# Performance work log

Measured on AMD Instinct MI355X. Metric: run time of the kernel, lower is better.

## Reference

```python
import jax, jax.numpy as jnp
import numpy as np

C0 = 0.28209479177387814
C1 = 0.4886025119029199
C2 = (1.0925484305920792, -1.0925484305920792, 0.31539156525252005,
      -1.0925484305920792, 0.5462742152960396)
EPS = 1e-6


def eval_sh_bases2(d):
    # d: [..., 3] unit directions -> [..., 9] SH basis (degree 2, svox2 convention)
    x, y, z = d[..., 0], d[..., 1], d[..., 2]
    return jnp.stack([
        jnp.full_like(x, C0),
        -C1 * y, C1 * z, -C1 * x,
        C2[0] * x * y, C2[1] * y * z,
        C2[2] * (2.0 * z * z - x * x - y * y),
        C2[3] * x * z, C2[4] * (x * x - y * y),
    ], axis=-1)


def get_sh_vals(xyz, sh_feats, invs, locs):
    # xyz: [N,3]; sh_feats: [J,9]; invs: [J,4,4]; locs: [J,3] -> weights [N,J]
    n = xyz.shape[0]
    xyz_h = jnp.concatenate([xyz, jnp.ones((n, 1), xyz.dtype)], axis=-1)  # [N,4]
    pts = jnp.einsum('jab,nb->jna', invs, xyz_h)[..., :3]  # [J,N,3]
    vd = locs[:, None, :] - pts                             # [J,N,3]
    norm = jnp.linalg.norm(vd, axis=-1)                     # [J,N]
    lengths = jnp.nan_to_num(norm)
    vd = vd / jnp.maximum(norm, 1e-12)[..., None]           # F.normalize
    sh = eval_sh_bases2(vd)                                 # [J,N,9]
    rads = jax.nn.relu(jnp.einsum('jnk,jk->jn', sh, sh_feats) + 0.5)
    rel = jax.nn.relu(1.0 - lengths / jnp.maximum(rads, EPS))
    rel = jnp.where(rads < EPS, 0.0, rel)
    return rel.T  # [N,J]


def weighted_transformation(pts, weights, transforms):
    # pts: [M,3]; weights: [M,J]; transforms: [J,4,4] (already inverse transforms,
    # if_transform_is_inv=True). Linear-blend the matrices and apply.
    wsum = weights.sum(axis=-1, keepdims=True)              # [M,1]
    wn = weights / jnp.maximum(wsum, EPS)
    T = jnp.einsum('mj,jab->mab', wn, transforms)           # [M,4,4]
    p_h = jnp.concatenate([pts, jnp.ones((pts.shape[0], 1), pts.dtype)], axis=-1)
    out = jnp.einsum('mab,mb->ma', T, p_h)[:, :3]
    return jnp.where(wsum > EPS, out, pts)                  # untouched if no weight


def setup_inputs() -> dict:
    key = jax.random.key(0)
    ks = jax.random.split(key, 5)
    B, S, J = 4096, 128, 24
    return {
        'xyz_sampled': jax.random.normal(ks[0], (B, S, 3), jnp.float32),
        'viewdirs': jax.random.normal(ks[1], (B, S, 3), jnp.float32),
        'transforms': jax.random.normal(ks[2], (J, 4, 4), jnp.float32),
        'ray_valid': jnp.ones((B, S), dtype=bool),
        'sh_feats': jax.random.normal(ks[3], (J, 9), jnp.float32),
        'locs': jax.random.normal(ks[4], (J, 3), jnp.float32),
    }


def reference(xyz_sampled, viewdirs, transforms, ray_valid, sh_feats, locs):
    shape = xyz_sampled.shape
    x = xyz_sampled.reshape(-1, 3)
    n = x.shape[0]
    tmp = jnp.concatenate([x, (xyz_sampled - viewdirs).reshape(-1, 3)], axis=0)  # [2N,3]
    w = get_sh_vals(x, sh_feats, transforms, locs)          # [N,J]
    w2 = jnp.concatenate([w, w], axis=0)                    # [2N,J]
    tmp = weighted_transformation(tmp, w2, transforms)      # [2N,3]
    xyz_out = tmp[:n]
    view_out = xyz_out - tmp[n:]
    return xyz_out.reshape(shape), view_out.reshape(shape)
```

## Files before the change

kernel.cpp:

```cpp
#include <hip/hip_runtime.h>

#define EPS 1e-6f
#define J 24
#define NPAIR 12
#define PAIR_STRIDE 56

typedef float v2f __attribute__((ext_vector_type(2)));

__device__ __forceinline__ v2f fma2(v2f a, v2f b, v2f c) {
    return __builtin_elementwise_fma(a, b, c);
}
__device__ __forceinline__ v2f max2(v2f a, v2f b) {
    return __builtin_elementwise_max(a, b);
}

__global__ void fold_kernel(const float* __restrict__ transforms,
                            const float* __restrict__ sh_feats,
                            const float* __restrict__ locs,
                            float* __restrict__ cj)
{
    const int j = threadIdx.x;
    if (j >= J) return;

    float F[9];
    #pragma unroll
    for (int k = 0; k < 9; ++k) F[k] = sh_feats[j * 9 + k];

    const float C0  = 0.28209479177387814f;
    const float C1  = 0.4886025119029199f;
    const float C2a = 1.0925484305920792f;

    const float f0  = C0 * F[0] + 0.5f;
    const float cy  = -C1 * F[1];
    const float cz  =  C1 * F[2];
    const float cx  = -C1 * F[3];
    const float cxy =  C2a * F[4];
    const float cyz = -C2a * F[5];
    const float c6  = 0.31539156525252005f * F[6];
    const float cxz = -C2a * F[7];
    const float c8  = 0.5462742152960396f  * F[8];

    float vals[25];
    #pragma unroll
    for (int k = 0; k < 12; ++k) vals[k] = transforms[j * 16 + k];
    vals[12] = locs[j * 3 + 0];
    vals[13] = locs[j * 3 + 1];
    vals[14] = locs[j * 3 + 2];
    vals[15] = f0;
    vals[16] = cx;  vals[17] = cy;  vals[18] = cz;
    vals[19] = cxy; vals[20] = cyz; vals[21] = cxz;
    vals[22] = c8 - c6;
    vals[23] = -c6 - c8;
    vals[24] = 2.0f * c6;

    float* base = cj + (j >> 1) * PAIR_STRIDE + (j & 1);
    #pragma unroll
    for (int k = 0; k < 25; ++k) base[2 * k] = vals[k];
}

__global__ __launch_bounds__(256, 8) void shcaster_kernel(
    const float* __restrict__ xyz,
    const float* __restrict__ vdir,
    const float* __restrict__ cj,
    float* __restrict__ out,
    int n)
{
    const int i = blockIdx.x * blockDim.x + threadIdx.x;
    if (i >= n) return;

    const float px = xyz[3 * i + 0];
    const float py = xyz[3 * i + 1];
    const float pz = xyz[3 * i + 2];
    const float vx = vdir[3 * i + 0];
    const float vy = vdir[3 * i + 1];
    const float vz = vdir[3 * i + 2];

    const v2f px2 = {px, px};
    const v2f py2 = {py, py};
    const v2f pz2 = {pz, pz};
    const v2f one2  = {1.f, 1.f};
    const v2f zero2 = {0.f, 0.f};

    v2f wsum2 = zero2;
    v2f Ta2[12];
    #pragma unroll
    for (int k = 0; k < 12; ++k) Ta2[k] = zero2;

    #pragma unroll 4
    for (int pp = 0; pp < NPAIR; ++pp) {
        const v2f* s = (const v2f*)(cj + pp * PAIR_STRIDE);

        const v2f ax = fma2(s[0], px2, fma2(s[1], py2, fma2(s[2],  pz2, s[3])));
        const v2f ay = fma2(s[4], px2, fma2(s[5], py2, fma2(s[6],  pz2, s[7])));
        const v2f az = fma2(s[8], px2, fma2(s[9], py2, fma2(s[10], pz2, s[11])));

        const v2f dx = s[12] - ax;
        const v2f dy = s[13] - ay;
        const v2f dz = s[14] - az;
        v2f d2 = fma2(dx, dx, fma2(dy, dy, dz * dz));
        d2 = max2(d2, (v2f){1e-24f, 1e-24f});

        const v2f inv = {__builtin_amdgcn_rsqf(d2.x), __builtin_amdgcn_rsqf(d2.y)};
        const v2f len = d2 * inv;
        const v2f nx = dx * inv;
        const v2f ny = dy * inv;
        const v2f nz = dz * inv;

        v2f rads = s[15];
        rads = fma2(s[16], nx, rads);
        rads = fma2(s[17], ny, rads);
        rads = fma2(s[18], nz, rads);
        rads = fma2(s[19], nx * ny, rads);
        rads = fma2(s[20], ny * nz, rads);
        rads = fma2(s[21], nx * nz, rads);
        rads = fma2(s[22], nx * nx, rads);
        rads = fma2(s[23], ny * ny, rads);
        rads = fma2(s[24], nz * nz, rads);
        rads = max2(rads, zero2);

        const v2f rc = {__builtin_amdgcn_rcpf(fmaxf(rads.x, EPS)),
                        __builtin_amdgcn_rcpf(fmaxf(rads.y, EPS))};
        v2f rel = max2(fma2(-len, rc, one2), zero2);
        rel.x = (rads.x < EPS) ? 0.f : rel.x;
        rel.y = (rads.y < EPS) ? 0.f : rel.y;

        wsum2 += rel;
        Ta2[0]  = fma2(rel, s[0],  Ta2[0]);
        Ta2[1]  = fma2(rel, s[1],  Ta2[1]);
        Ta2[2]  = fma2(rel, s[2],  Ta2[2]);
        Ta2[3]  = fma2(rel, s[3],  Ta2[3]);
        Ta2[4]  = fma2(rel, s[4],  Ta2[4]);
        Ta2[5]  = fma2(rel, s[5],  Ta2[5]);
        Ta2[6]  = fma2(rel, s[6],  Ta2[6]);
        Ta2[7]  = fma2(rel, s[7],  Ta2[7]);
        Ta2[8]  = fma2(rel, s[8],  Ta2[8]);
        Ta2[9]  = fma2(rel, s[9],  Ta2[9]);
        Ta2[10] = fma2(rel, s[10], Ta2[10]);
        Ta2[11] = fma2(rel, s[11], Ta2[11]);
    }

    const float wsum = wsum2.x + wsum2.y;
    float Ta[12];
    #pragma unroll
    for (int k = 0; k < 12; ++k) Ta[k] = Ta2[k].x + Ta2[k].y;

    const float inv_w = __builtin_amdgcn_rcpf(fmaxf(wsum, EPS));
    const bool valid = wsum > EPS;

    const float axo = fmaf(Ta[0], px, fmaf(Ta[1], py, fmaf(Ta[2],  pz, Ta[3])))  * inv_w;
    const float ayo = fmaf(Ta[4], px, fmaf(Ta[5], py, fmaf(Ta[6],  pz, Ta[7])))  * inv_w;
    const float azo = fmaf(Ta[8], px, fmaf(Ta[9], py, fmaf(Ta[10], pz, Ta[11]))) * inv_w;

    const float qx = px - vx;
    const float qy = py - vy;
    const float qz = pz - vz;
    const float bxo = fmaf(Ta[0], qx, fmaf(Ta[1], qy, fmaf(Ta[2],  qz, Ta[3])))  * inv_w;
    const float byo = fmaf(Ta[4], qx, fmaf(Ta[5], qy, fmaf(Ta[6],  qz, Ta[7])))  * inv_w;
    const float bzo = fmaf(Ta[8], qx, fmaf(Ta[9], qy, fmaf(Ta[10], qz, Ta[11]))) * inv_w;

    const float ox = valid ? axo : px;
    const float oy = valid ? ayo : py;
    const float oz = valid ? azo : pz;
    const float wx = ox - (valid ? bxo : qx);
    const float wy = oy - (valid ? byo : qy);
    const float wz = oz - (valid ? bzo : qz);

    out[3 * i + 0] = ox;
    out[3 * i + 1] = oy;
    out[3 * i + 2] = oz;
    float* out2 = out + (size_t)3 * n;
    out2[3 * i + 0] = wx;
    out2[3 * i + 1] = wy;
    out2[3 * i + 2] = wz;
}

extern "C" void kernel_launch(void* const* d_in, const int* in_sizes, int n_in,
                              void* d_out, int out_size, void* d_ws, size_t ws_size,
                              hipStream_t stream) {
    const int n = (out_size > 0) ? (out_size / 6) : 524288;
    const int big = 3 * n;

    const float* xyz  = nullptr;
    const float* vdir = nullptr;
    const float* trf  = nullptr;
    const float* shf  = nullptr;
    const float* locs = nullptr;
    int bigSeen = 0;
    for (int k = 0; k < n_in; ++k) {
        const int s = in_sizes[k];
        if (s == big) {
            if (bigSeen++ == 0) xyz = (const float*)d_in[k];
            else                vdir = (const float*)d_in[k];
        } else if (s == 384) {
            trf = (const float*)d_in[k];
        } else if (s == 216) {
            shf = (const float*)d_in[k];
        } else if (s == 72) {
            locs = (const float*)d_in[k];
        }
    }
    if (!xyz || !vdir || !trf || !shf || !locs) {
        xyz  = (const float*)d_in[0];
        vdir = (const float*)d_in[1];
        trf  = (const float*)d_in[2];
        shf  = (const float*)d_in[n_in >= 6 ? 4 : 3];
        locs = (const float*)d_in[n_in >= 6 ? 5 : 4];
    }

    float* cj = (float*)d_ws;
    float* out = (float*)d_out;

    fold_kernel<<<1, 64, 0, stream>>>(trf, shf, locs, cj);

    const int block = 256;
    const int grid = (n + block - 1) / block;
    shcaster_kernel<<<grid, block, 0, stream>>>(xyz, vdir, cj, out, n);
}
```

Before: 89.75 us.

## Process two points per thread to amortize joint-constant loads

Each thread now handles two points (g and g+n/2) and evaluates every joint pair for both, so each uniform constant load feeds twice the arithmetic. The SH radius polynomial is split into three partial accumulators to shorten the dependent FMA chain. The vdir loads move after the joint loop, launch bounds drop to 4 waves per SIMD, and the grid is halved. In exchange the kernel uses more registers and less occupancy, and an odd n would leave the last point unprocessed.

```diff
diff --git a/kernel.cpp b/kernel.cpp
--- a/kernel.cpp
+++ b/kernel.cpp
@@ -58,120 +58,131 @@
     for (int k = 0; k < 25; ++k) base[2 * k] = vals[k];
 }
 
-__global__ __launch_bounds__(256, 8) void shcaster_kernel(
+struct PState {
+    float px, py, pz;
+    v2f wsum2;
+    v2f Ta2[12];
+};
+
+__device__ __forceinline__ void joint_pair(const v2f* __restrict__ s, PState& st) {
+    const v2f px2 = {st.px, st.px};
+    const v2f py2 = {st.py, st.py};
+    const v2f pz2 = {st.pz, st.pz};
+    const v2f one2  = {1.f, 1.f};
+    const v2f zero2 = {0.f, 0.f};
+
+    const v2f ax = fma2(s[0], px2, fma2(s[1], py2, fma2(s[2],  pz2, s[3])));
+    const v2f ay = fma2(s[4], px2, fma2(s[5], py2, fma2(s[6],  pz2, s[7])));
+    const v2f az = fma2(s[8], px2, fma2(s[9], py2, fma2(s[10], pz2, s[11])));
+
+    const v2f dx = s[12] - ax;
+    const v2f dy = s[13] - ay;
+    const v2f dz = s[14] - az;
+    v2f d2 = fma2(dx, dx, fma2(dy, dy, dz * dz));
+    d2 = max2(d2, (v2f){1e-24f, 1e-24f});
+
+    const v2f inv = {__builtin_amdgcn_rsqf(d2.x), __builtin_amdgcn_rsqf(d2.y)};
+    const v2f len = d2 * inv;
+    const v2f nx = dx * inv;
+    const v2f ny = dy * inv;
+    const v2f nz = dz * inv;
+
+    v2f r0 = fma2(s[16], nx, s[15]);
+    r0 = fma2(s[19], nx * ny, r0);
+    r0 = fma2(s[22], nx * nx, r0);
+    v2f r1 = fma2(s[17], ny, zero2);
+    r1 = fma2(s[20], ny * nz, r1);
+    r1 = fma2(s[23], ny * ny, r1);
+    v2f r2 = fma2(s[18], nz, zero2);
+    r2 = fma2(s[21], nx * nz, r2);
+    r2 = fma2(s[24], nz * nz, r2);
+    v2f rads = (r0 + r1) + r2;
+    rads = max2(rads, zero2);
+
+    const v2f rc = {__builtin_amdgcn_rcpf(fmaxf(rads.x, EPS)),
+                    __builtin_amdgcn_rcpf(fmaxf(rads.y, EPS))};
+    v2f rel = max2(fma2(-len, rc, one2), zero2);
+    rel.x = (rads.x < EPS) ? 0.f : rel.x;
+    rel.y = (rads.y < EPS) ? 0.f : rel.y;
+
+    st.wsum2 += rel;
+    #pragma unroll
+    for (int k = 0; k < 12; ++k) st.Ta2[k] = fma2(rel, s[k], st.Ta2[k]);
+}
+
+__device__ __forceinline__ void finish_store(const PState& st,
+                                             float vx, float vy, float vz,
+                                             float* __restrict__ out,
+                                             float* __restrict__ out2, int i) {
+    const float wsum = st.wsum2.x + st.wsum2.y;
+    float Ta[12];
+    #pragma unroll
+    for (int k = 0; k < 12; ++k) Ta[k] = st.Ta2[k].x + st.Ta2[k].y;
+
+    const float inv_w = __builtin_amdgcn_rcpf(fmaxf(wsum, EPS));
+    const bool valid = wsum > EPS;
+    const float px = st.px, py = st.py, pz = st.pz;
+
+    const float axo = fmaf(Ta[0], px, fmaf(Ta[1], py, fmaf(Ta[2],  pz, Ta[3])))  * inv_w;
+    const float ayo = fmaf(Ta[4], px, fmaf(Ta[5], py, fmaf(Ta[6],  pz, Ta[7])))  * inv_w;
+    const float azo = fmaf(Ta[8], px, fmaf(Ta[9], py, fmaf(Ta[10], pz, Ta[11]))) * inv_w;
+
+    const float qx = px - vx;
+    const float qy = py - vy;
+    const float qz = pz - vz;
+    const float bxo = fmaf(Ta[0], qx, fmaf(Ta[1], qy, fmaf(Ta[2],  qz, Ta[3])))  * inv_w;
+    const float byo = fmaf(Ta[4], qx, fmaf(Ta[5], qy, fmaf(Ta[6],  qz, Ta[7])))  * inv_w;
+    const float bzo = fmaf(Ta[8], qx, fmaf(Ta[9], qy, fmaf(Ta[10], qz, Ta[11]))) * inv_w;
+
+    const float ox = valid ? axo : px;
+    const float oy = valid ? ayo : py;
+    const float oz = valid ? azo : pz;
+    const float wx = ox - (valid ? bxo : qx);
+    const float wy = oy - (valid ? byo : qy);
+    const float wz = oz - (valid ? bzo : qz);
+
+    out[3 * i + 0] = ox;
+    out[3 * i + 1] = oy;
+    out[3 * i + 2] = oz;
+    out2[3 * i + 0] = wx;
+    out2[3 * i + 1] = wy;
+    out2[3 * i + 2] = wz;
+}
+
+__global__ __launch_bounds__(256, 4) void shcaster_kernel(
     const float* __restrict__ xyz,
     const float* __restrict__ vdir,
     const float* __restrict__ cj,
     float* __restrict__ out,
     int n)
 {
-    const int i = blockIdx.x * blockDim.x + threadIdx.x;
-    if (i >= n) return;
-
-    const float px = xyz[3 * i + 0];
-    const float py = xyz[3 * i + 1];
-    const float pz = xyz[3 * i + 2];
-    const float vx = vdir[3 * i + 0];
-    const float vy = vdir[3 * i + 1];
-    const float vz = vdir[3 * i + 2];
-
-    const v2f px2 = {px, px};
-    const v2f py2 = {py, py};
-    const v2f pz2 = {pz, pz};
-    const v2f one2  = {1.f, 1.f};
-    const v2f zero2 = {0.f, 0.f};
-
-    v2f wsum2 = zero2;
-    v2f Ta2[12];
-    #pragma unroll
-    for (int k = 0; k < 12; ++k) Ta2[k] = zero2;
-
-    #pragma unroll 4
+    const int n2 = n >> 1;
+    const int g = blockIdx.x * blockDim.x + threadIdx.x;
+    if (g >= n2) return;
+    const int ia = g;
+    const int ib = g + n2;
+
+    PState A, B;
+    A.px = xyz[3 * ia + 0]; A.py = xyz[3 * ia + 1]; A.pz = xyz[3 * ia + 2];
+    B.px = xyz[3 * ib + 0]; B.py = xyz[3 * ib + 1]; B.pz = xyz[3 * ib + 2];
+    A.wsum2 = (v2f){0.f, 0.f};
+    B.wsum2 = (v2f){0.f, 0.f};
+    #pragma unroll
+    for (int k = 0; k < 12; ++k) { A.Ta2[k] = (v2f){0.f, 0.f}; B.Ta2[k] = (v2f){0.f, 0.f}; }
+
+    #pragma unroll 2
     for (int pp = 0; pp < NPAIR; ++pp) {
         const v2f* s = (const v2f*)(cj + pp * PAIR_STRIDE);
-
-        const v2f ax = fma2(s[0], px2, fma2(s[1], py2, fma2(s[2],  pz2, s[3])));
-        const v2f ay = fma2(s[4], px2, fma2(s[5], py2, fma2(s[6],  pz2, s[7])));
-        const v2f az = fma2(s[8], px2, fma2(s[9], py2, fma2(s[10], pz2, s[11])));
-
-        const v2f dx = s[12] - ax;
-        const v2f dy = s[13] - ay;
-        const v2f dz = s[14] - az;
-        v2f d2 = fma2(dx, dx, fma2(dy, dy, dz * dz));
-        d2 = max2(d2, (v2f){1e-24f, 1e-24f});
-
-        const v2f inv = {__builtin_amdgcn_rsqf(d2.x), __builtin_amdgcn_rsqf(d2.y)};
-        const v2f len = d2 * inv;
-        const v2f nx = dx * inv;
-        const v2f ny = dy * inv;
-        const v2f nz = dz * inv;
-
-        v2f rads = s[15];
-        rads = fma2(s[16], nx, rads);
-        rads = fma2(s[17], ny, rads);
-        rads = fma2(s[18], nz, rads);
-        rads = fma2(s[19], nx * ny, rads);
-        rads = fma2(s[20], ny * nz, rads);
-        rads = fma2(s[21], nx * nz, rads);
-        rads = fma2(s[22], nx * nx, rads);
-        rads = fma2(s[23], ny * ny, rads);
-        rads = fma2(s[24], nz * nz, rads);
-        rads = max2(rads, zero2);
-
-        const v2f rc = {__builtin_amdgcn_rcpf(fmaxf(rads.x, EPS)),
-                        __builtin_amdgcn_rcpf(fmaxf(rads.y, EPS))};
-        v2f rel = max2(fma2(-len, rc, one2), zero2);
-        rel.x = (rads.x < EPS) ? 0.f : rel.x;
-        rel.y = (rads.y < EPS) ? 0.f : rel.y;
-
-        wsum2 += rel;
-        Ta2[0]  = fma2(rel, s[0],  Ta2[0]);
-        Ta2[1]  = fma2(rel, s[1],  Ta2[1]);
-        Ta2[2]  = fma2(rel, s[2],  Ta2[2]);
-        Ta2[3]  = fma2(rel, s[3],  Ta2[3]);
-        Ta2[4]  = fma2(rel, s[4],  Ta2[4]);
-        Ta2[5]  = fma2(rel, s[5],  Ta2[5]);
-        Ta2[6]  = fma2(rel, s[6],  Ta2[6]);
-        Ta2[7]  = fma2(rel, s[7],  Ta2[7]);
-        Ta2[8]  = fma2(rel, s[8],  Ta2[8]);
-        Ta2[9]  = fma2(rel, s[9],  Ta2[9]);
-        Ta2[10] = fma2(rel, s[10], Ta2[10]);
-        Ta2[11] = fma2(rel, s[11], Ta2[11]);
+        joint_pair(s, A);
+        joint_pair(s, B);
     }
 
-    const float wsum = wsum2.x + wsum2.y;
-    float Ta[12];
-    #pragma unroll
-    for (int k = 0; k < 12; ++k) Ta[k] = Ta2[k].x + Ta2[k].y;
-
-    const float inv_w = __builtin_amdgcn_rcpf(fmaxf(wsum, EPS));
-    const bool valid = wsum > EPS;
-
-    const float axo = fmaf(Ta[0], px, fmaf(Ta[1], py, fmaf(Ta[2],  pz, Ta[3])))  * inv_w;
-    const float ayo = fmaf(Ta[4], px, fmaf(Ta[5], py, fmaf(Ta[6],  pz, Ta[7])))  * inv_w;
-    const float azo = fmaf(Ta[8], px, fmaf(Ta[9], py, fmaf(Ta[10], pz, Ta[11]))) * inv_w;
-
-    const float qx = px - vx;
-    const float qy = py - vy;
-    const float qz = pz - vz;
-    const float bxo = fmaf(Ta[0], qx, fmaf(Ta[1], qy, fmaf(Ta[2],  qz, Ta[3])))  * inv_w;
-    const float byo = fmaf(Ta[4], qx, fmaf(Ta[5], qy, fmaf(Ta[6],  qz, Ta[7])))  * inv_w;
-    const float bzo = fmaf(Ta[8], qx, fmaf(Ta[9], qy, fmaf(Ta[10], qz, Ta[11]))) * inv_w;
-
-    const float ox = valid ? axo : px;
-    const float oy = valid ? ayo : py;
-    const float oz = valid ? azo : pz;
-    const float wx = ox - (valid ? bxo : qx);
-    const float wy = oy - (valid ? byo : qy);
-    const float wz = oz - (valid ? bzo : qz);
-
-    out[3 * i + 0] = ox;
-    out[3 * i + 1] = oy;
-    out[3 * i + 2] = oz;
+    const float vxa = vdir[3 * ia + 0], vya = vdir[3 * ia + 1], vza = vdir[3 * ia + 2];
+    const float vxb = vdir[3 * ib + 0], vyb = vdir[3 * ib + 1], vzb = vdir[3 * ib + 2];
+
     float* out2 = out + (size_t)3 * n;
-    out2[3 * i + 0] = wx;
-    out2[3 * i + 1] = wy;
-    out2[3 * i + 2] = wz;
+    finish_store(A, vxa, vya, vza, out, out2, ia);
+    finish_store(B, vxb, vyb, vzb, out, out2, ib);
 }
 
 extern "C" void kernel_launch(void* const* d_in, const int* in_sizes, int n_in,
@@ -212,7 +223,8 @@
 
     fold_kernel<<<1, 64, 0, stream>>>(trf, shf, locs, cj);
 
+    const int n2 = n >> 1;
     const int block = 256;
-    const int grid = (n + block - 1) / block;
+    const int grid = (n2 + block - 1) / block;
     shcaster_kernel<<<grid, block, 0, stream>>>(xyz, vdir, cj, out, n);
 }
```

New measurement: 89.36 us. About the same (-0.4%).
